# Optimization experiments

Hardware: AMD Instinct MI355X
Metric: run time of the kernel (lower is better)

The kernel has to match this reference:

```python
import jax, jax.numpy as jnp
import numpy as np

K = 3          # kernel_size
PAD = 1        # padding for offset conv and deform conv
UPS = 2        # ConvTranspose2d stride
EPS = 1e-5     # BatchNorm eps


def _conv2d(x, w, b, pad):
    y = jax.lax.conv_general_dilated(x, w, (1, 1), [(pad, pad), (pad, pad)],
                                     dimension_numbers=('NCHW', 'OIHW', 'NCHW'))
    return y + b[None, :, None, None]


def _deform_conv(x, offsets, w, b):
    # torchvision DeformConv2d semantics, stride=1, pad=1, dilation=1
    B, C, H, W = x.shape
    KK = K * K
    off = offsets.reshape(B, KK, 2, H, W)  # [:, kk, 0]=dy, [:, kk, 1]=dx
    ki, kj = jnp.meshgrid(jnp.arange(K), jnp.arange(K), indexing='ij')
    py = (jnp.arange(H) - PAD)[None, None, :, None] + ki.ravel()[None, :, None, None] + off[:, :, 0]
    px = (jnp.arange(W) - PAD)[None, None, None, :] + kj.ravel()[None, :, None, None] + off[:, :, 1]
    y0f = jnp.floor(py); x0f = jnp.floor(px)
    ly = py - y0f; lx = px - x0f
    y0 = y0f.astype(jnp.int32); x0 = x0f.astype(jnp.int32)
    xf = x.reshape(B, C, H * W)

    def corner(yy, xx, wgt):
        valid = (yy >= 0) & (yy < H) & (xx >= 0) & (xx < W)
        idx = jnp.clip(yy, 0, H - 1) * W + jnp.clip(xx, 0, W - 1)      # [B,KK,H,W]
        v = jax.vmap(lambda f, i: f[:, i])(xf, idx)                     # [B,C,KK,H,W]
        return v * (wgt * valid)[:, None]

    s = (corner(y0, x0, (1 - ly) * (1 - lx)) + corner(y0, x0 + 1, (1 - ly) * lx)
         + corner(y0 + 1, x0, ly * (1 - lx)) + corner(y0 + 1, x0 + 1, ly * lx))
    out = jnp.einsum('bckhw,ock->bohw', s, w.reshape(w.shape[0], C, KK))
    return out + b[None, :, None, None]


def _conv_transpose(x, w, b):
    # torch ConvTranspose2d(stride=UPS, padding=0); torch weight is [C_in, C_out, K, K]
    wf = jnp.flip(jnp.transpose(w, (1, 0, 2, 3)), (2, 3))
    y = jax.lax.conv_general_dilated(x, wf, (1, 1), [(K - 1, K - 1)] * 2,
                                     lhs_dilation=(UPS, UPS),
                                     dimension_numbers=('NCHW', 'OIHW', 'NCHW'))
    return y + b[None, :, None, None]


def setup_inputs() -> dict:
    key = jax.random.key(0)
    ks = jax.random.split(key, 8)
    B, Cin, Cout, H, W = 16, 64, 128, 64, 64
    s = 0.05
    return {
        'x': jax.random.normal(ks[0], (B, Cin, H, W), jnp.float32),
        'w_off': jax.random.normal(ks[1], (2 * K * K, Cin, K, K), jnp.float32) * s,
        'b_off': jax.random.normal(ks[2], (2 * K * K,), jnp.float32) * s,
        'w_def': jax.random.normal(ks[3], (Cout, Cin, K, K), jnp.float32) * s,
        'b_def': jax.random.normal(ks[4], (Cout,), jnp.float32) * s,
        'w_up': jax.random.normal(ks[5], (Cout, Cout, K, K), jnp.float32) * s,
        'b_up': jax.random.normal(ks[6], (Cout,), jnp.float32) * s,
        'gamma': jnp.ones((Cout,), jnp.float32),
        'beta': jnp.zeros((Cout,), jnp.float32),
    }


def reference(x, w_off, b_off, w_def, b_def, w_up, b_up, gamma, beta):
    offsets = _conv2d(x, w_off, b_off, PAD)
    feats = _deform_conv(x, offsets, w_def, b_def)
    y = _conv_transpose(feats, w_up, b_up)
    # BatchNorm2d (training mode, biased batch stats) + ReLU
    mu = jnp.mean(y, axis=(0, 2, 3), keepdims=True)
    var = jnp.var(y, axis=(0, 2, 3), keepdims=True)
    yn = (y - mu) * jax.lax.rsqrt(var + EPS)
    yn = yn * gamma[None, :, None, None] + beta[None, :, None, None]
    return jax.nn.relu(yn)
```

## Files before the change

### kernel.cpp

```cpp
#include <hip/hip_runtime.h>
#include <math.h>

#define PADC 1
#define CIN  64
#define COUT 128
#define IH   64
#define IW   64
#define NB   16
#define OYX  129
#define OXP  136
#define NOFF 18
#define SPO  (OYX * OYX)
#define BNEPS 1e-5f
#define NBLK_CT (NB * 65)

typedef __attribute__((ext_vector_type(8))) short bf16x8;
typedef __attribute__((ext_vector_type(4))) float f32x4;

static __device__ __forceinline__ unsigned short f2bf(float f) {
    unsigned int b = __float_as_uint(f);
    unsigned int r = (b + 0x7FFFu + ((b >> 16) & 1u)) >> 16;
    return (unsigned short)r;
}
static __device__ __forceinline__ float bf2f(unsigned short u) {
    return __uint_as_float((unsigned int)u << 16);
}

__global__ void k_prep(const float* __restrict__ w_def, const float* __restrict__ w_up,
                       const float* __restrict__ w_off,
                       unsigned short* __restrict__ WDF, unsigned short* __restrict__ WB,
                       unsigned short* __restrict__ WOF)
{
    int idx = blockIdx.x * 256 + threadIdx.x;
    if (idx < 73728) {
        const int j = idx & 7;
        const int n = (idx >> 3) & 127;
        const int g = idx >> 10;
        const int kg = g & 3, ks = (g >> 2) & 1, kk = g >> 3;
        const int c = ks * 32 + kg * 8 + j;
        WDF[idx] = f2bf(w_def[(n * CIN + c) * 9 + kk]);
    }
    const int i2 = idx - 73728;
    if (i2 >= 0 && i2 < 147456) {
        const int j = i2 & 7;
        const int n = (i2 >> 3) & 127;
        int ky, kx, ci;
        if (i2 < 65536) {
            const int k = (i2 >> 10) * 8 + j;
            ky = (k >> 8) ? 0 : 2;
            kx = ((k >> 7) & 1) ? 0 : 2;
            ci = k & 127;
        } else if (i2 < 98304) {
            const int k = ((i2 - 65536) >> 10) * 8 + j;
            ky = 1;
            kx = (k >> 7) ? 0 : 2;
            ci = k & 127;
        } else if (i2 < 131072) {
            const int k = ((i2 - 98304) >> 10) * 8 + j;
            ky = (k >> 7) ? 0 : 2;
            kx = 1;
            ci = k & 127;
        } else {
            const int k = ((i2 - 131072) >> 10) * 8 + j;
            ky = 1; kx = 1;
            ci = k & 127;
        }
        WB[i2] = f2bf(w_up[((ci * COUT + n) * 3 + ky) * 3 + kx]);
    }
    const int i3 = idx - 221184;
    if (i3 >= 0 && i3 < 18432) {
        const int j = i3 & 7;
        const int n = (i3 >> 3) & 31;
        const int g = i3 >> 8;
        const int kg = g & 3, s = g >> 2;
        const int c  = (s & 1) * 32 + kg * 8 + j;
        const int kk = s >> 1;
        const int ki = kk / 3, kj = kk - 3 * ki;
        WOF[i3] = (n < NOFF) ? f2bf(w_off[((n * CIN + c) * 3 + ki) * 3 + kj]) : (unsigned short)0;
    }
}

__global__ __launch_bounds__(256) void k_xt(const float* __restrict__ x, unsigned short* __restrict__ xt)
{
    __shared__ unsigned short t[64][66];
    const int tid = threadIdx.x;
    const int h = blockIdx.x & 63, b = blockIdx.x >> 6;
    const int w = tid & 63, cq = tid >> 6;
    #pragma unroll
    for (int p = 0; p < 16; ++p) {
        const int c = p * 4 + cq;
        t[w][c] = f2bf(x[((size_t)((b * 64 + c) * 64) + h) * 64 + w]);
    }
    __syncthreads();
    const int w2 = tid >> 2, q = tid & 3;
    unsigned int pk[8];
    #pragma unroll
    for (int m = 0; m < 8; ++m)
        pk[m] = (unsigned int)t[w2][q * 16 + 2 * m] | ((unsigned int)t[w2][q * 16 + 2 * m + 1] << 16);
    uint4* dst = (uint4*)(xt + ((size_t)((b * 64 + h) * 64) + w2) * 64 + q * 16);
    dst[0] = uint4{pk[0], pk[1], pk[2], pk[3]};
    dst[1] = uint4{pk[4], pk[5], pk[6], pk[7]};
}

__global__ __launch_bounds__(64, 4) void k_offset_mfma(
    const unsigned short* __restrict__ xt, const unsigned short* __restrict__ WOF,
    const float* __restrict__ b_off, float* __restrict__ offs)
{
    const int l  = threadIdx.x;
    const int ml = l & 15;
    const int kg = l >> 4;
    const int q  = blockIdx.x & 3;
    const int h  = (blockIdx.x >> 2) & 63;
    const int b  = blockIdx.x >> 8;
    const int w  = q * 16 + ml;
    const unsigned short* xb = xt + (size_t)b * (IH * IW * CIN);

    const f32x4 fz = {0.f, 0.f, 0.f, 0.f};
    f32x4 acc0 = fz, acc1 = fz;

    #pragma unroll 1
    for (int s = 0; s < 18; ++s) {
        const int kk = s >> 1;
        const int ki = kk / 3, kj = kk - 3 * ki;
        const int c0 = (s & 1) * 32 + kg * 8;
        const int yy = h - PADC + ki;
        const int xx = w - PADC + kj;
        const bf16x8 b0 = *(const bf16x8*)(WOF + (size_t)(((s * 4 + kg) * 32 + ml) * 8));
        const bf16x8 b1 = *(const bf16x8*)(WOF + (size_t)(((s * 4 + kg) * 32 + 16 + ml) * 8));
        bf16x8 a = {0, 0, 0, 0, 0, 0, 0, 0};
        if (yy >= 0 && yy < IH && xx >= 0 && xx < IW)
            a = *(const bf16x8*)(xb + (size_t)((yy * IW + xx) * CIN) + c0);
        acc0 = __builtin_amdgcn_mfma_f32_16x16x32_bf16(a, b0, acc0, 0, 0, 0);
        acc1 = __builtin_amdgcn_mfma_f32_16x16x32_bf16(a, b1, acc1, 0, 0, 0);
    }
    #pragma unroll
    for (int nt = 0; nt < 2; ++nt) {
        const int oc = nt * 16 + ml;
        if (oc < NOFF) {
            const float bias = b_off[oc];
            const f32x4 av = nt ? acc1 : acc0;
            #pragma unroll
            for (int j = 0; j < 4; ++j) {
                const int wd = q * 16 + kg * 4 + j;
                offs[((size_t)(b * NOFF + oc) * IH + h) * IW + wd] = av[j] + bias;
            }
        }
    }
}

__global__ __launch_bounds__(64, 4) void k_deform_mfma(
    const unsigned short* __restrict__ xt, const float* __restrict__ offs,
    const unsigned short* __restrict__ WDF, const float* __restrict__ b_def,
    unsigned short* __restrict__ feats_bf)
{
    const int l  = threadIdx.x;
    const int ml = l & 15;
    const int kg = l >> 4;
    const int q  = blockIdx.x & 3;
    const int h  = (blockIdx.x >> 2) & 63;
    const int b  = blockIdx.x >> 8;
    const int w  = q * 16 + ml;

    const unsigned short* xb = xt + (size_t)b * (IH * IW * CIN);

    const f32x4 fz = {0.f, 0.f, 0.f, 0.f};
    f32x4 acc[8];
    #pragma unroll
    for (int nt = 0; nt < 8; ++nt) acc[nt] = fz;

    #pragma unroll 1
    for (int kk = 0; kk < 9; ++kk) {
        const int ki = kk / 3, kj = kk - 3 * ki;
        const float dy = offs[((b * NOFF + 2 * kk) * IH + h) * IW + w];
        const float dx = offs[((b * NOFF + 2 * kk + 1) * IH + h) * IW + w];
        const float py = (float)(h - PADC + ki) + dy;
        const float px = (float)(w - PADC + kj) + dx;
        const float y0f = floorf(py), x0f = floorf(px);
        const float ly = py - y0f, lx = px - x0f;
        const int y0 = (int)y0f, x0 = (int)x0f;
        const float wy[2] = {1.f - ly, ly};
        const float wx[2] = {1.f - lx, lx};
        int   cidx[4];
        float cwgt[4];
        #pragma unroll
        for (int cy = 0; cy < 2; ++cy)
            #pragma unroll
            for (int cx = 0; cx < 2; ++cx) {
                const int yy = y0 + cy, xx = x0 + cx;
                const bool v = (yy >= 0) & (yy < IH) & (xx >= 0) & (xx < IW);
                cidx[cy * 2 + cx] = v ? ((yy * IW + xx) * CIN) : 0;
                cwgt[cy * 2 + cx] = v ? (wy[cy] * wx[cx]) : 0.f;
            }
        #pragma unroll
        for (int ks = 0; ks < 2; ++ks) {
            const int c0 = ks * 32 + kg * 8;
            uint4 cv[4];
            #pragma unroll
            for (int cp = 0; cp < 4; ++cp)
                cv[cp] = *(const uint4*)(xb + cidx[cp] + c0);
            bf16x8 bfr[8];
            #pragma unroll
            for (int nt = 0; nt < 8; ++nt)
                bfr[nt] = *(const bf16x8*)(WDF + ((size_t)((kk * 8 + ks * 4 + kg) * 128) + nt * 16 + ml) * 8);
            float sf[8] = {0.f, 0.f, 0.f, 0.f, 0.f, 0.f, 0.f, 0.f};
            #pragma unroll
            for (int cp = 0; cp < 4; ++cp) {
                const float wg = cwgt[cp];
                const unsigned int u0 = cv[cp].x, u1 = cv[cp].y, u2 = cv[cp].z, u3 = cv[cp].w;
                sf[0] += wg * __uint_as_float(u0 << 16);
                sf[1] += wg * __uint_as_float(u0 & 0xFFFF0000u);
                sf[2] += wg * __uint_as_float(u1 << 16);
                sf[3] += wg * __uint_as_float(u1 & 0xFFFF0000u);
                sf[4] += wg * __uint_as_float(u2 << 16);
                sf[5] += wg * __uint_as_float(u2 & 0xFFFF0000u);
                sf[6] += wg * __uint_as_float(u3 << 16);
                sf[7] += wg * __uint_as_float(u3 & 0xFFFF0000u);
            }
            union { unsigned short us[8]; bf16x8 v; } pa;
            #pragma unroll
            for (int j = 0; j < 8; ++j) pa.us[j] = f2bf(sf[j]);
            #pragma unroll
            for (int nt = 0; nt < 8; ++nt)
                acc[nt] = __builtin_amdgcn_mfma_f32_16x16x32_bf16(pa.v, bfr[nt], acc[nt], 0, 0, 0);
        }
    }
    #pragma unroll
    for (int nt = 0; nt < 8; ++nt) {
        const int o = nt * 16 + ml;
        const float bias = b_def[o];
        #pragma unroll
        for (int j = 0; j < 4; ++j) {
            const int wd = q * 16 + kg * 4 + j;
            feats_bf[((size_t)((b * IH + h) * IW) + wd) * COUT + o] = f2bf(acc[nt][j] + bias);
        }
    }
}

__global__ __launch_bounds__(256) void k_convT_mfma(
    const unsigned short* __restrict__ feats_bf, const unsigned short* __restrict__ WB,
    unsigned short* __restrict__ y_bf, float* __restrict__ partials)
{
    __shared__ __align__(16) char smem[33792];

    const int tid = threadIdx.x;
    const int l   = tid & 63;
    const int wv  = tid >> 6;
    const int ml  = l & 15;
    const int kg  = l >> 4;
    const int blk = blockIdx.x;
    const int t   = blk % 65;
    const int b   = blk / 65;

    for (int r = 0; r < 2; ++r) {
        char* dstbase = smem + r * 16896;
        const int iy = t - 1 + r;
        if (iy < 0 || iy > 63) {
            for (int i = tid; i < 1056; i += 256)
                *(uint4*)(dstbase + i * 16) = uint4{0, 0, 0, 0};
        } else {
            const unsigned short* src = feats_bf + (size_t)(b * IH + iy) * (IW * COUT);
            for (int i = tid; i < 1024; i += 256) {
                const uint4 v = *(const uint4*)(src + i * 8);
                const int G = 16 + i;
                const int phys = G ^ ((G >> 4) & 7);
                *(uint4*)(dstbase + phys * 16) = v;
            }
            if (tid < 32) {
                const int G = (tid < 16) ? tid : (1024 + tid);
                const int phys = G ^ ((G >> 4) & 7);
                *(uint4*)(dstbase + phys * 16) = uint4{0, 0, 0, 0};
            }
        }
    }
    __syncthreads();

    const int n0 = wv * 32;
    const f32x4 fz = {0.f, 0.f, 0.f, 0.f};
    float sacc[2] = {0.f, 0.f}, qacc[2] = {0.f, 0.f};

    #pragma unroll 1
    for (int p = 0; p < 2; ++p) {
        if (p == 1 && t == 64) break;
        const int oy = 2 * t + p;
        const unsigned short* segG0 = WB + (p ? 65536 : 0);
        const unsigned short* segG1 = WB + (p ? 131072 : 98304);
        const int nK0 = p ? 8 : 16;
        const int nK1 = p ? 4 : 8;

        f32x4 acc0[5][2], acc1[4][2];
        #pragma unroll
        for (int m = 0; m < 5; ++m) { acc0[m][0] = fz; acc0[m][1] = fz; }
        #pragma unroll
        for (int m = 0; m < 4; ++m) { acc1[m][0] = fz; acc1[m][1] = fz; }

        for (int ks = 0; ks < nK0; ++ks) {
            const int kk   = ks * 32 + kg * 8;
            const int slot = p ? 1 : (kk >> 8);
            const int kb   = (kk & 255) >> 3;
            const bf16x8 b0 = *(const bf16x8*)(segG0 + ((ks * 4 + kg) * 128 + n0 + ml) * 8);
            const bf16x8 b1 = *(const bf16x8*)(segG0 + ((ks * 4 + kg) * 128 + n0 + 16 + ml) * 8);
            #pragma unroll
            for (int mt = 0; mt < 5; ++mt) {
                int tx = mt * 16 + ml; if (tx > 64) tx = 64;
                const int G = tx * 16 + kb;
                const int phys = G ^ ((G >> 4) & 7);
                const bf16x8 a = *(const bf16x8*)(smem + slot * 16896 + phys * 16);
                acc0[mt][0] = __builtin_amdgcn_mfma_f32_16x16x32_bf16(a, b0, acc0[mt][0], 0, 0, 0);
                acc0[mt][1] = __builtin_amdgcn_mfma_f32_16x16x32_bf16(a, b1, acc0[mt][1], 0, 0, 0);
            }
        }
        for (int ks = 0; ks < nK1; ++ks) {
            const int kk   = ks * 32 + kg * 8;
            const int slot = p ? 1 : (kk >> 7);
            const int kb   = (kk & 127) >> 3;
            const bf16x8 b0 = *(const bf16x8*)(segG1 + ((ks * 4 + kg) * 128 + n0 + ml) * 8);
            const bf16x8 b1 = *(const bf16x8*)(segG1 + ((ks * 4 + kg) * 128 + n0 + 16 + ml) * 8);
            #pragma unroll
            for (int mt = 0; mt < 4; ++mt) {
                const int tx = mt * 16 + ml;
                const int G = 16 + tx * 16 + kb;
                const int phys = G ^ ((G >> 4) & 7);
                const bf16x8 a = *(const bf16x8*)(smem + slot * 16896 + phys * 16);
                acc1[mt][0] = __builtin_amdgcn_mfma_f32_16x16x32_bf16(a, b0, acc1[mt][0], 0, 0, 0);
                acc1[mt][1] = __builtin_amdgcn_mfma_f32_16x16x32_bf16(a, b1, acc1[mt][1], 0, 0, 0);
            }
        }

        #pragma unroll
        for (int nt = 0; nt < 2; ++nt) {
            const int co = n0 + nt * 16 + ml;
            unsigned int* drow32 = (unsigned int*)(y_bf + ((size_t)(b * COUT + co) * OYX + oy) * OXP);
            #pragma unroll
            for (int mt = 0; mt < 4; ++mt) {
                unsigned int pk[4];
                #pragma unroll
                for (int j = 0; j < 4; ++j) {
                    const float ve = acc0[mt][nt][j];
                    const float vo = acc1[mt][nt][j];
                    pk[j] = (unsigned int)f2bf(ve) | ((unsigned int)f2bf(vo) << 16);
                    sacc[nt] += ve + vo;
                    qacc[nt] += ve * ve + vo * vo;
                }
                *(uint4*)(drow32 + mt * 16 + kg * 4) = uint4{pk[0], pk[1], pk[2], pk[3]};
            }
            if (kg == 0) {
                const float ve = acc0[4][nt][0];
                drow32[64] = (unsigned int)f2bf(ve);
                sacc[nt] += ve;
                qacc[nt] += ve * ve;
            }
        }
    }

    #pragma unroll
    for (int nt = 0; nt < 2; ++nt) {
        float ss = sacc[nt], qq = qacc[nt];
        ss += __shfl_xor(ss, 16, 64); qq += __shfl_xor(qq, 16, 64);
        ss += __shfl_xor(ss, 32, 64); qq += __shfl_xor(qq, 32, 64);
        if (kg == 0) {
            float* pp = partials + ((size_t)blk * COUT + n0 + nt * 16 + ml) * 2;
            pp[0] = ss; pp[1] = qq;
        }
    }
}

__global__ __launch_bounds__(256) void k_bn_final(const float* __restrict__ partials,
                                                  float* __restrict__ stats)
{
    const int c = blockIdx.x;
    const int tid = threadIdx.x;
    float s = 0.f, q = 0.f;
    for (int i = tid; i < NBLK_CT; i += 256) {
        const float* pp = partials + ((size_t)i * COUT + c) * 2;
        s += pp[0]; q += pp[1];
    }
    __shared__ float rs[256], rq[256];
    rs[tid] = s; rq[tid] = q;
    __syncthreads();
    for (int off = 128; off > 0; off >>= 1) {
        if (tid < off) { rs[tid] += rs[tid + off]; rq[tid] += rq[tid + off]; }
        __syncthreads();
    }
    if (tid == 0) {
        const float n = (float)(NB * SPO);
        const float mean = rs[0] / n;
        const float var  = rq[0] / n - mean * mean;
        stats[c] = mean;
        stats[COUT + c] = rsqrtf(var + BNEPS);
    }
}

__global__ __launch_bounds__(256) void k_bn_apply(
    const unsigned short* __restrict__ y_bf, float* __restrict__ y,
    const float* __restrict__ stats,
    const float* __restrict__ gamma, const float* __restrict__ beta)
{
    const int v = blockIdx.x * 256 + threadIdx.x;
    const int rid = v / 17;
    const int c   = v - rid * 17;
    const int co  = (rid / OYX) & (COUT - 1);
    const float mean = stats[co], rstd = stats[COUT + co];
    const float ga = gamma[co], be = beta[co];
    const int ox0 = c * 8;

    const uint4 u = *(const uint4*)(y_bf + (size_t)rid * OXP + ox0);
    const unsigned int uu[4] = {u.x, u.y, u.z, u.w};
    float* dst = y + (size_t)rid * OYX + ox0;
    const int nv = (c < 16) ? 8 : 1;
    #pragma unroll
    for (int m = 0; m < 4; ++m) {
        float v0 = bf2f((unsigned short)(uu[m] & 0xFFFFu));
        float v1 = bf2f((unsigned short)(uu[m] >> 16));
        v0 = fmaxf((v0 - mean) * rstd * ga + be, 0.f);
        v1 = fmaxf((v1 - mean) * rstd * ga + be, 0.f);
        if (2 * m < nv)     dst[2 * m]     = v0;
        if (2 * m + 1 < nv) dst[2 * m + 1] = v1;
    }
}

extern "C" void kernel_launch(void* const* d_in, const int* in_sizes, int n_in,
                              void* d_out, int out_size, void* d_ws, size_t ws_size,
                              hipStream_t stream)
{
    const float* x     = (const float*)d_in[0];
    const float* w_off = (const float*)d_in[1];
    const float* b_off = (const float*)d_in[2];
    const float* w_def = (const float*)d_in[3];
    const float* b_def = (const float*)d_in[4];
    const float* w_up  = (const float*)d_in[5];
    const float* b_up  = (const float*)d_in[6];  (void)b_up;
    const float* gamma = (const float*)d_in[7];
    const float* beta  = (const float*)d_in[8];
    float* y = (float*)d_out;

    float* ws       = (float*)d_ws;
    float* offs     = ws;
    float* stats    = offs + 1179648;
    float* partials = stats + 256;
    unsigned short* xt       = (unsigned short*)(partials + 528384);
    unsigned short* WDF      = xt + 4194304;
    unsigned short* feats_bf = WDF + 73728;
    unsigned short* WB       = feats_bf + 8388608;
    unsigned short* WOF      = WB + 147456;
    unsigned short* y_bf     = WOF + 18432;

    k_prep        <<<dim3(936),    dim3(256), 0, stream>>>(w_def, w_up, w_off, WDF, WB, WOF);
    k_xt          <<<dim3(1024),   dim3(256), 0, stream>>>(x, xt);
    k_offset_mfma <<<dim3(4096),   dim3(64),  0, stream>>>(xt, WOF, b_off, offs);
    k_deform_mfma <<<dim3(4096),   dim3(64),  0, stream>>>(xt, offs, WDF, b_def, feats_bf);
    k_convT_mfma  <<<dim3(NBLK_CT),dim3(256), 0, stream>>>(feats_bf, WB, y_bf, partials);
    k_bn_final    <<<dim3(128),    dim3(256), 0, stream>>>(partials, stats);
    k_bn_apply    <<<dim3(17544),  dim3(256), 0, stream>>>(y_bf, y, stats, gamma, beta);
}
```

Measured before the change: 174.9 us.

## Fuse offset conv into deform conv and merge weight prep with input transpose

Merges the weight-prep and input-transpose kernels into one launch, and fuses the offset convolution into the deformable convolution. Offsets now stay in shared memory instead of round-tripping through a global buffer. Each deform block now uses two waves that split the 64 input channels and combine partial accumulators through shared memory. The offset conv is computed redundantly by both waves, and the extra LDS reduction and barrier add cost in exchange for fewer launches and less global traffic.

```diff
diff --git a/kernel.cpp b/kernel.cpp
--- a/kernel.cpp
+++ b/kernel.cpp
@@ -26,12 +26,34 @@
     return __uint_as_float((unsigned int)u << 16);
 }
 
-__global__ void k_prep(const float* __restrict__ w_def, const float* __restrict__ w_up,
-                       const float* __restrict__ w_off,
-                       unsigned short* __restrict__ WDF, unsigned short* __restrict__ WB,
-                       unsigned short* __restrict__ WOF)
-{
-    int idx = blockIdx.x * 256 + threadIdx.x;
+__global__ __launch_bounds__(256) void k_pre(
+    const float* __restrict__ x, const float* __restrict__ w_def,
+    const float* __restrict__ w_up, const float* __restrict__ w_off,
+    unsigned short* __restrict__ xt, unsigned short* __restrict__ WDF,
+    unsigned short* __restrict__ WB, unsigned short* __restrict__ WOF)
+{
+    __shared__ unsigned short t[64][66];
+    const int tid = threadIdx.x;
+    if (blockIdx.x < 1024) {
+        const int h = blockIdx.x & 63, b = blockIdx.x >> 6;
+        const int w = tid & 63, cq = tid >> 6;
+        #pragma unroll
+        for (int p = 0; p < 16; ++p) {
+            const int c = p * 4 + cq;
+            t[w][c] = f2bf(x[((size_t)((b * 64 + c) * 64) + h) * 64 + w]);
+        }
+        __syncthreads();
+        const int w2 = tid >> 2, q = tid & 3;
+        unsigned int pk[8];
+        #pragma unroll
+        for (int m = 0; m < 8; ++m)
+            pk[m] = (unsigned int)t[w2][q * 16 + 2 * m] | ((unsigned int)t[w2][q * 16 + 2 * m + 1] << 16);
+        uint4* dst = (uint4*)(xt + ((size_t)((b * 64 + h) * 64) + w2) * 64 + q * 16);
+        dst[0] = uint4{pk[0], pk[1], pk[2], pk[3]};
+        dst[1] = uint4{pk[4], pk[5], pk[6], pk[7]};
+        return;
+    }
+    int idx = (blockIdx.x - 1024) * 256 + tid;
     if (idx < 73728) {
         const int j = idx & 7;
         const int n = (idx >> 3) & 127;
@@ -80,99 +102,68 @@
     }
 }
 
-__global__ __launch_bounds__(256) void k_xt(const float* __restrict__ x, unsigned short* __restrict__ xt)
-{
-    __shared__ unsigned short t[64][66];
+__global__ __launch_bounds__(128, 6) void k_deform_fused(
+    const unsigned short* __restrict__ xt, const unsigned short* __restrict__ WOF,
+    const float* __restrict__ b_off, const unsigned short* __restrict__ WDF,
+    const float* __restrict__ b_def, unsigned short* __restrict__ feats_bf)
+{
     const int tid = threadIdx.x;
-    const int h = blockIdx.x & 63, b = blockIdx.x >> 6;
-    const int w = tid & 63, cq = tid >> 6;
-    #pragma unroll
-    for (int p = 0; p < 16; ++p) {
-        const int c = p * 4 + cq;
-        t[w][c] = f2bf(x[((size_t)((b * 64 + c) * 64) + h) * 64 + w]);
+    const int ws  = tid >> 6;
+    const int l   = tid & 63;
+    const int ml  = l & 15;
+    const int kg  = l >> 4;
+    const int u   = blockIdx.x;
+    const int q   = u & 3;
+    const int h   = (u >> 2) & 63;
+    const int b   = u >> 8;
+    const int w   = q * 16 + ml;
+    const unsigned short* xb = xt + (size_t)b * (IH * IW * CIN);
+
+    __shared__ float off_lds[2][16][19];
+    __shared__ f32x4 red[2][4][64];
+
+    const f32x4 fz = {0.f, 0.f, 0.f, 0.f};
+
+    {
+        f32x4 oa0 = fz, oa1 = fz;
+        #pragma unroll 1
+        for (int s = 0; s < 18; ++s) {
+            const int kk = s >> 1;
+            const int ki = kk / 3, kj = kk - 3 * ki;
+            const int c0 = (s & 1) * 32 + kg * 8;
+            const int yy = h - PADC + ki;
+            const int xx = w - PADC + kj;
+            const bf16x8 b0 = *(const bf16x8*)(WOF + (size_t)(((s * 4 + kg) * 32 + ml) * 8));
+            const bf16x8 b1 = *(const bf16x8*)(WOF + (size_t)(((s * 4 + kg) * 32 + 16 + ml) * 8));
+            bf16x8 a = {0, 0, 0, 0, 0, 0, 0, 0};
+            if (yy >= 0 && yy < IH && xx >= 0 && xx < IW)
+                a = *(const bf16x8*)(xb + (size_t)((yy * IW + xx) * CIN) + c0);
+            oa0 = __builtin_amdgcn_mfma_f32_16x16x32_bf16(a, b0, oa0, 0, 0, 0);
+            oa1 = __builtin_amdgcn_mfma_f32_16x16x32_bf16(a, b1, oa1, 0, 0, 0);
+        }
+        const float bo0 = b_off[ml];
+        #pragma unroll
+        for (int j = 0; j < 4; ++j)
+            off_lds[ws][kg * 4 + j][ml] = oa0[j] + bo0;
+        if (ml < 2) {
+            const float bo1 = b_off[16 + ml];
+            #pragma unroll
+            for (int j = 0; j < 4; ++j)
+                off_lds[ws][kg * 4 + j][16 + ml] = oa1[j] + bo1;
+        }
     }
     __syncthreads();
-    const int w2 = tid >> 2, q = tid & 3;
-    unsigned int pk[8];
-    #pragma unroll
-    for (int m = 0; m < 8; ++m)
-        pk[m] = (unsigned int)t[w2][q * 16 + 2 * m] | ((unsigned int)t[w2][q * 16 + 2 * m + 1] << 16);
-    uint4* dst = (uint4*)(xt + ((size_t)((b * 64 + h) * 64) + w2) * 64 + q * 16);
-    dst[0] = uint4{pk[0], pk[1], pk[2], pk[3]};
-    dst[1] = uint4{pk[4], pk[5], pk[6], pk[7]};
-}
-
-__global__ __launch_bounds__(64, 4) void k_offset_mfma(
-    const unsigned short* __restrict__ xt, const unsigned short* __restrict__ WOF,
-    const float* __restrict__ b_off, float* __restrict__ offs)
-{
-    const int l  = threadIdx.x;
-    const int ml = l & 15;
-    const int kg = l >> 4;
-    const int q  = blockIdx.x & 3;
-    const int h  = (blockIdx.x >> 2) & 63;
-    const int b  = blockIdx.x >> 8;
-    const int w  = q * 16 + ml;
-    const unsigned short* xb = xt + (size_t)b * (IH * IW * CIN);
-
-    const f32x4 fz = {0.f, 0.f, 0.f, 0.f};
-    f32x4 acc0 = fz, acc1 = fz;
-
-    #pragma unroll 1
-    for (int s = 0; s < 18; ++s) {
-        const int kk = s >> 1;
-        const int ki = kk / 3, kj = kk - 3 * ki;
-        const int c0 = (s & 1) * 32 + kg * 8;
-        const int yy = h - PADC + ki;
-        const int xx = w - PADC + kj;
-        const bf16x8 b0 = *(const bf16x8*)(WOF + (size_t)(((s * 4 + kg) * 32 + ml) * 8));
-        const bf16x8 b1 = *(const bf16x8*)(WOF + (size_t)(((s * 4 + kg) * 32 + 16 + ml) * 8));
-        bf16x8 a = {0, 0, 0, 0, 0, 0, 0, 0};
-        if (yy >= 0 && yy < IH && xx >= 0 && xx < IW)
-            a = *(const bf16x8*)(xb + (size_t)((yy * IW + xx) * CIN) + c0);
-        acc0 = __builtin_amdgcn_mfma_f32_16x16x32_bf16(a, b0, acc0, 0, 0, 0);
-        acc1 = __builtin_amdgcn_mfma_f32_16x16x32_bf16(a, b1, acc1, 0, 0, 0);
-    }
-    #pragma unroll
-    for (int nt = 0; nt < 2; ++nt) {
-        const int oc = nt * 16 + ml;
-        if (oc < NOFF) {
-            const float bias = b_off[oc];
-            const f32x4 av = nt ? acc1 : acc0;
-            #pragma unroll
-            for (int j = 0; j < 4; ++j) {
-                const int wd = q * 16 + kg * 4 + j;
-                offs[((size_t)(b * NOFF + oc) * IH + h) * IW + wd] = av[j] + bias;
-            }
-        }
-    }
-}
-
-__global__ __launch_bounds__(64, 4) void k_deform_mfma(
-    const unsigned short* __restrict__ xt, const float* __restrict__ offs,
-    const unsigned short* __restrict__ WDF, const float* __restrict__ b_def,
-    unsigned short* __restrict__ feats_bf)
-{
-    const int l  = threadIdx.x;
-    const int ml = l & 15;
-    const int kg = l >> 4;
-    const int q  = blockIdx.x & 3;
-    const int h  = (blockIdx.x >> 2) & 63;
-    const int b  = blockIdx.x >> 8;
-    const int w  = q * 16 + ml;
-
-    const unsigned short* xb = xt + (size_t)b * (IH * IW * CIN);
-
-    const f32x4 fz = {0.f, 0.f, 0.f, 0.f};
+
     f32x4 acc[8];
     #pragma unroll
     for (int nt = 0; nt < 8; ++nt) acc[nt] = fz;
+    const int c0 = ws * 32 + kg * 8;
 
     #pragma unroll 1
     for (int kk = 0; kk < 9; ++kk) {
         const int ki = kk / 3, kj = kk - 3 * ki;
-        const float dy = offs[((b * NOFF + 2 * kk) * IH + h) * IW + w];
-        const float dx = offs[((b * NOFF + 2 * kk + 1) * IH + h) * IW + w];
+        const float dy = off_lds[ws][ml][2 * kk];
+        const float dx = off_lds[ws][ml][2 * kk + 1];
         const float py = (float)(h - PADC + ki) + dy;
         const float px = (float)(w - PADC + kj) + dx;
         const float y0f = floorf(py), x0f = floorf(px);
@@ -191,47 +182,55 @@
                 cidx[cy * 2 + cx] = v ? ((yy * IW + xx) * CIN) : 0;
                 cwgt[cy * 2 + cx] = v ? (wy[cy] * wx[cx]) : 0.f;
             }
-        #pragma unroll
-        for (int ks = 0; ks < 2; ++ks) {
-            const int c0 = ks * 32 + kg * 8;
-            uint4 cv[4];
-            #pragma unroll
-            for (int cp = 0; cp < 4; ++cp)
-                cv[cp] = *(const uint4*)(xb + cidx[cp] + c0);
-            bf16x8 bfr[8];
-            #pragma unroll
-            for (int nt = 0; nt < 8; ++nt)
-                bfr[nt] = *(const bf16x8*)(WDF + ((size_t)((kk * 8 + ks * 4 + kg) * 128) + nt * 16 + ml) * 8);
-            float sf[8] = {0.f, 0.f, 0.f, 0.f, 0.f, 0.f, 0.f, 0.f};
-            #pragma unroll
-            for (int cp = 0; cp < 4; ++cp) {
-                const float wg = cwgt[cp];
-                const unsigned int u0 = cv[cp].x, u1 = cv[cp].y, u2 = cv[cp].z, u3 = cv[cp].w;
-                sf[0] += wg * __uint_as_float(u0 << 16);
-                sf[1] += wg * __uint_as_float(u0 & 0xFFFF0000u);
-                sf[2] += wg * __uint_as_float(u1 << 16);
-                sf[3] += wg * __uint_as_float(u1 & 0xFFFF0000u);
-                sf[4] += wg * __uint_as_float(u2 << 16);
-                sf[5] += wg * __uint_as_float(u2 & 0xFFFF0000u);
-                sf[6] += wg * __uint_as_float(u3 << 16);
-                sf[7] += wg * __uint_as_float(u3 & 0xFFFF0000u);
-            }
-            union { unsigned short us[8]; bf16x8 v; } pa;
-            #pragma unroll
-            for (int j = 0; j < 8; ++j) pa.us[j] = f2bf(sf[j]);
-            #pragma unroll
-            for (int nt = 0; nt < 8; ++nt)
-                acc[nt] = __builtin_amdgcn_mfma_f32_16x16x32_bf16(pa.v, bfr[nt], acc[nt], 0, 0, 0);
-        }
-    }
+        uint4 cv[4];
+        #pragma unroll
+        for (int cp = 0; cp < 4; ++cp)
+            cv[cp] = *(const uint4*)(xb + cidx[cp] + c0);
+        float sf[8] = {0.f, 0.f, 0.f, 0.f, 0.f, 0.f, 0.f, 0.f};
+        #pragma unroll
+        for (int cp = 0; cp < 4; ++cp) {
+            const float wg = cwgt[cp];
+            const unsigned int u0 = cv[cp].x, u1 = cv[cp].y, u2 = cv[cp].z, u3 = cv[cp].w;
+            sf[0] += wg * __uint_as_float(u0 << 16);
+            sf[1] += wg * __uint_as_float(u0 & 0xFFFF0000u);
+            sf[2] += wg * __uint_as_float(u1 << 16);
+            sf[3] += wg * __uint_as_float(u1 & 0xFFFF0000u);
+            sf[4] += wg * __uint_as_float(u2 << 16);
+            sf[5] += wg * __uint_as_float(u2 & 0xFFFF0000u);
+            sf[6] += wg * __uint_as_float(u3 << 16);
+            sf[7] += wg * __uint_as_float(u3 & 0xFFFF0000u);
+        }
+        union { unsigned short us[8]; bf16x8 v; } pa;
+        #pragma unroll
+        for (int j = 0; j < 8; ++j) pa.us[j] = f2bf(sf[j]);
+        #pragma unroll
+        for (int half = 0; half < 2; ++half) {
+            bf16x8 bfr[4];
+            #pragma unroll
+            for (int nn = 0; nn < 4; ++nn)
+                bfr[nn] = *(const bf16x8*)(WDF + ((size_t)((kk * 8 + ws * 4 + kg) * 128) + (half * 4 + nn) * 16 + ml) * 8);
+            #pragma unroll
+            for (int nn = 0; nn < 4; ++nn)
+                acc[half * 4 + nn] = __builtin_amdgcn_mfma_f32_16x16x32_bf16(pa.v, bfr[nn], acc[half * 4 + nn], 0, 0, 0);
+        }
+    }
+
+    const int oth = 1 - ws;
     #pragma unroll
-    for (int nt = 0; nt < 8; ++nt) {
+    for (int nn = 0; nn < 4; ++nn)
+        red[oth][nn][l] = acc[oth * 4 + nn];
+    __syncthreads();
+    #pragma unroll
+    for (int nn = 0; nn < 4; ++nn) {
+        const int nt = ws * 4 + nn;
+        const f32x4 r2 = red[ws][nn][l];
         const int o = nt * 16 + ml;
         const float bias = b_def[o];
         #pragma unroll
         for (int j = 0; j < 4; ++j) {
             const int wd = q * 16 + kg * 4 + j;
-            feats_bf[((size_t)((b * IH + h) * IW) + wd) * COUT + o] = f2bf(acc[nt][j] + bias);
+            feats_bf[((size_t)((b * IH + h) * IW) + wd) * COUT + o] =
+                f2bf(acc[nt][j] + r2[j] + bias);
         }
     }
 }
@@ -434,8 +433,7 @@
     float* y = (float*)d_out;
 
     float* ws       = (float*)d_ws;
-    float* offs     = ws;
-    float* stats    = offs + 1179648;
+    float* stats    = ws;
     float* partials = stats + 256;
     unsigned short* xt       = (unsigned short*)(partials + 528384);
     unsigned short* WDF      = xt + 4194304;
@@ -444,11 +442,9 @@
     unsigned short* WOF      = WB + 147456;
     unsigned short* y_bf     = WOF + 18432;
 
-    k_prep        <<<dim3(936),    dim3(256), 0, stream>>>(w_def, w_up, w_off, WDF, WB, WOF);
-    k_xt          <<<dim3(1024),   dim3(256), 0, stream>>>(x, xt);
-    k_offset_mfma <<<dim3(4096),   dim3(64),  0, stream>>>(xt, WOF, b_off, offs);
-    k_deform_mfma <<<dim3(4096),   dim3(64),  0, stream>>>(xt, offs, WDF, b_def, feats_bf);
-    k_convT_mfma  <<<dim3(NBLK_CT),dim3(256), 0, stream>>>(feats_bf, WB, y_bf, partials);
-    k_bn_final    <<<dim3(128),    dim3(256), 0, stream>>>(partials, stats);
-    k_bn_apply    <<<dim3(17544),  dim3(256), 0, stream>>>(y_bf, y, stats, gamma, beta);
-}
+    k_pre          <<<dim3(1960),   dim3(256), 0, stream>>>(x, w_def, w_up, w_off, xt, WDF, WB, WOF);
+    k_deform_fused <<<dim3(4096),   dim3(128), 0, stream>>>(xt, WOF, b_off, WDF, b_def, feats_bf);
+    k_convT_mfma   <<<dim3(NBLK_CT),dim3(256), 0, stream>>>(feats_bf, WB, y_bf, partials);
+    k_bn_final     <<<dim3(128),    dim3(256), 0, stream>>>(partials, stats);
+    k_bn_apply     <<<dim3(17544),  dim3(256), 0, stream>>>(y_bf, y, stats, gamma, beta);
+}
```

After: 266.0 us. 1.52x slower.

## Merge prep kernels, store offsets pixel-major, unroll deform loop with split weight loads

Applied to the files above, without the earlier changes.

Fuses the bf16 transpose of x and the weight-repacking kernel into a single launch, removing one kernel launch. Offsets are now written pixel-major (18 contiguous floats per pixel), so the deform kernel preloads all nine dy/dx pairs up front as float2 loads instead of issuing strided scalar loads inside the loop. The deform kk loop is fully unrolled, and the weight fragments are loaded in two halves of four to keep register pressure down. The offset writes become strided across pixels, and full unrolling may raise register use and hurt occupancy.

```diff
diff --git a/kernel.cpp b/kernel.cpp
--- a/kernel.cpp
+++ b/kernel.cpp
@@ -26,12 +26,34 @@
     return __uint_as_float((unsigned int)u << 16);
 }
 
-__global__ void k_prep(const float* __restrict__ w_def, const float* __restrict__ w_up,
-                       const float* __restrict__ w_off,
-                       unsigned short* __restrict__ WDF, unsigned short* __restrict__ WB,
-                       unsigned short* __restrict__ WOF)
-{
-    int idx = blockIdx.x * 256 + threadIdx.x;
+__global__ __launch_bounds__(256) void k_pre(
+    const float* __restrict__ x, const float* __restrict__ w_def,
+    const float* __restrict__ w_up, const float* __restrict__ w_off,
+    unsigned short* __restrict__ xt, unsigned short* __restrict__ WDF,
+    unsigned short* __restrict__ WB, unsigned short* __restrict__ WOF)
+{
+    __shared__ unsigned short t[64][66];
+    const int tid = threadIdx.x;
+    if (blockIdx.x < 1024) {
+        const int h = blockIdx.x & 63, b = blockIdx.x >> 6;
+        const int w = tid & 63, cq = tid >> 6;
+        #pragma unroll
+        for (int p = 0; p < 16; ++p) {
+            const int c = p * 4 + cq;
+            t[w][c] = f2bf(x[((size_t)((b * 64 + c) * 64) + h) * 64 + w]);
+        }
+        __syncthreads();
+        const int w2 = tid >> 2, q = tid & 3;
+        unsigned int pk[8];
+        #pragma unroll
+        for (int m = 0; m < 8; ++m)
+            pk[m] = (unsigned int)t[w2][q * 16 + 2 * m] | ((unsigned int)t[w2][q * 16 + 2 * m + 1] << 16);
+        uint4* dst = (uint4*)(xt + ((size_t)((b * 64 + h) * 64) + w2) * 64 + q * 16);
+        dst[0] = uint4{pk[0], pk[1], pk[2], pk[3]};
+        dst[1] = uint4{pk[4], pk[5], pk[6], pk[7]};
+        return;
+    }
+    int idx = (blockIdx.x - 1024) * 256 + tid;
     if (idx < 73728) {
         const int j = idx & 7;
         const int n = (idx >> 3) & 127;
@@ -80,31 +102,9 @@
     }
 }
 
-__global__ __launch_bounds__(256) void k_xt(const float* __restrict__ x, unsigned short* __restrict__ xt)
-{
-    __shared__ unsigned short t[64][66];
-    const int tid = threadIdx.x;
-    const int h = blockIdx.x & 63, b = blockIdx.x >> 6;
-    const int w = tid & 63, cq = tid >> 6;
-    #pragma unroll
-    for (int p = 0; p < 16; ++p) {
-        const int c = p * 4 + cq;
-        t[w][c] = f2bf(x[((size_t)((b * 64 + c) * 64) + h) * 64 + w]);
-    }
-    __syncthreads();
-    const int w2 = tid >> 2, q = tid & 3;
-    unsigned int pk[8];
-    #pragma unroll
-    for (int m = 0; m < 8; ++m)
-        pk[m] = (unsigned int)t[w2][q * 16 + 2 * m] | ((unsigned int)t[w2][q * 16 + 2 * m + 1] << 16);
-    uint4* dst = (uint4*)(xt + ((size_t)((b * 64 + h) * 64) + w2) * 64 + q * 16);
-    dst[0] = uint4{pk[0], pk[1], pk[2], pk[3]};
-    dst[1] = uint4{pk[4], pk[5], pk[6], pk[7]};
-}
-
 __global__ __launch_bounds__(64, 4) void k_offset_mfma(
     const unsigned short* __restrict__ xt, const unsigned short* __restrict__ WOF,
-    const float* __restrict__ b_off, float* __restrict__ offs)
+    const float* __restrict__ b_off, float* __restrict__ offs2)
 {
     const int l  = threadIdx.x;
     const int ml = l & 15;
@@ -142,14 +142,14 @@
             #pragma unroll
             for (int j = 0; j < 4; ++j) {
                 const int wd = q * 16 + kg * 4 + j;
-                offs[((size_t)(b * NOFF + oc) * IH + h) * IW + wd] = av[j] + bias;
+                offs2[((size_t)((b * IH + h) * IW) + wd) * NOFF + oc] = av[j] + bias;
             }
         }
     }
 }
 
 __global__ __launch_bounds__(64, 4) void k_deform_mfma(
-    const unsigned short* __restrict__ xt, const float* __restrict__ offs,
+    const unsigned short* __restrict__ xt, const float* __restrict__ offs2,
     const unsigned short* __restrict__ WDF, const float* __restrict__ b_def,
     unsigned short* __restrict__ feats_bf)
 {
@@ -163,18 +163,24 @@
 
     const unsigned short* xb = xt + (size_t)b * (IH * IW * CIN);
 
+    float2 dd[9];
+    {
+        const float* op = offs2 + ((size_t)((b * IH + h) * IW) + w) * NOFF;
+        #pragma unroll
+        for (int kk = 0; kk < 9; ++kk)
+            dd[kk] = *(const float2*)(op + 2 * kk);
+    }
+
     const f32x4 fz = {0.f, 0.f, 0.f, 0.f};
     f32x4 acc[8];
     #pragma unroll
     for (int nt = 0; nt < 8; ++nt) acc[nt] = fz;
 
-    #pragma unroll 1
+    #pragma unroll
     for (int kk = 0; kk < 9; ++kk) {
         const int ki = kk / 3, kj = kk - 3 * ki;
-        const float dy = offs[((b * NOFF + 2 * kk) * IH + h) * IW + w];
-        const float dx = offs[((b * NOFF + 2 * kk + 1) * IH + h) * IW + w];
-        const float py = (float)(h - PADC + ki) + dy;
-        const float px = (float)(w - PADC + kj) + dx;
+        const float py = (float)(h - PADC + ki) + dd[kk].x;
+        const float px = (float)(w - PADC + kj) + dd[kk].y;
         const float y0f = floorf(py), x0f = floorf(px);
         const float ly = py - y0f, lx = px - x0f;
         const int y0 = (int)y0f, x0 = (int)x0f;
@@ -198,10 +204,6 @@
             #pragma unroll
             for (int cp = 0; cp < 4; ++cp)
                 cv[cp] = *(const uint4*)(xb + cidx[cp] + c0);
-            bf16x8 bfr[8];
-            #pragma unroll
-            for (int nt = 0; nt < 8; ++nt)
-                bfr[nt] = *(const bf16x8*)(WDF + ((size_t)((kk * 8 + ks * 4 + kg) * 128) + nt * 16 + ml) * 8);
             float sf[8] = {0.f, 0.f, 0.f, 0.f, 0.f, 0.f, 0.f, 0.f};
             #pragma unroll
             for (int cp = 0; cp < 4; ++cp) {
@@ -220,8 +222,15 @@
             #pragma unroll
             for (int j = 0; j < 8; ++j) pa.us[j] = f2bf(sf[j]);
             #pragma unroll
-            for (int nt = 0; nt < 8; ++nt)
-                acc[nt] = __builtin_amdgcn_mfma_f32_16x16x32_bf16(pa.v, bfr[nt], acc[nt], 0, 0, 0);
+            for (int half = 0; half < 2; ++half) {
+                bf16x8 bfr[4];
+                #pragma unroll
+                for (int nn = 0; nn < 4; ++nn)
+                    bfr[nn] = *(const bf16x8*)(WDF + ((size_t)((kk * 8 + ks * 4 + kg) * 128) + (half * 4 + nn) * 16 + ml) * 8);
+                #pragma unroll
+                for (int nn = 0; nn < 4; ++nn)
+                    acc[half * 4 + nn] = __builtin_amdgcn_mfma_f32_16x16x32_bf16(pa.v, bfr[nn], acc[half * 4 + nn], 0, 0, 0);
+            }
         }
     }
     #pragma unroll
@@ -434,21 +443,20 @@
     float* y = (float*)d_out;
 
     float* ws       = (float*)d_ws;
-    float* offs     = ws;
-    float* stats    = offs + 1179648;
+    float* stats    = ws;
     float* partials = stats + 256;
-    unsigned short* xt       = (unsigned short*)(partials + 528384);
+    float* offs2    = partials + 528384;
+    unsigned short* xt       = (unsigned short*)(offs2 + 1179648);
     unsigned short* WDF      = xt + 4194304;
     unsigned short* feats_bf = WDF + 73728;
     unsigned short* WB       = feats_bf + 8388608;
     unsigned short* WOF      = WB + 147456;
     unsigned short* y_bf     = WOF + 18432;
 
-    k_prep        <<<dim3(936),    dim3(256), 0, stream>>>(w_def, w_up, w_off, WDF, WB, WOF);
-    k_xt          <<<dim3(1024),   dim3(256), 0, stream>>>(x, xt);
-    k_offset_mfma <<<dim3(4096),   dim3(64),  0, stream>>>(xt, WOF, b_off, offs);
-    k_deform_mfma <<<dim3(4096),   dim3(64),  0, stream>>>(xt, offs, WDF, b_def, feats_bf);
-    k_convT_mfma  <<<dim3(NBLK_CT),dim3(256), 0, stream>>>(feats_bf, WB, y_bf, partials);
-    k_bn_final    <<<dim3(128),    dim3(256), 0, stream>>>(partials, stats);
-    k_bn_apply    <<<dim3(17544),  dim3(256), 0, stream>>>(y_bf, y, stats, gamma, beta);
-}
+    k_pre          <<<dim3(1960),   dim3(256), 0, stream>>>(x, w_def, w_up, w_off, xt, WDF, WB, WOF);
+    k_offset_mfma  <<<dim3(4096),   dim3(64),  0, stream>>>(xt, WOF, b_off, offs2);
+    k_deform_mfma  <<<dim3(4096),   dim3(64),  0, stream>>>(xt, offs2, WDF, b_def, feats_bf);
+    k_convT_mfma   <<<dim3(NBLK_CT),dim3(256), 0, stream>>>(feats_bf, WB, y_bf, partials);
+    k_bn_final     <<<dim3(128),    dim3(256), 0, stream>>>(partials, stats);
+    k_bn_apply     <<<dim3(17544),  dim3(256), 0, stream>>>(y_bf, y, stats, gamma, beta);
+}
```

Result: faster. 161.7 us (-7.5%).
